# Kernel optimization log

Measured on AMD Instinct MI355X. Metric: run time of the kernel, lower is better.

The kernel has to match this reference:

```python
import math
import jax, jax.numpy as jnp
import numpy as np

B, N, D = 16, 2048, 128
MASK_VALUE = -1000000.0


def setup_inputs() -> dict:
    key = jax.random.key(0)
    k1, k2, k3, k4 = jax.random.split(key, 4)
    queries = jax.random.normal(k1, (B, N, D), dtype=jnp.float32)
    keys = jax.random.normal(k2, (B, N, D), dtype=jnp.float32)
    values = jax.random.normal(k3, (B, N, D), dtype=jnp.float32)
    valid_lens = jax.random.randint(k4, (B,), 0, N, dtype=jnp.int32)
    return {"queries": queries, "keys": keys, "values": values, "valid_lens": valid_lens}


def reference(queries, keys, values, valid_lens):
    d = queries.shape[-1]
    # [B, Nq, Nk] full score matrix, as in the original bmm
    scores = jnp.einsum("bqd,bkd->bqk", queries, keys) / math.sqrt(d)
    # Faithful to the source bug: valid_lens.dim (a method) != 1, so it is
    # flattened and scores[idx][valid_len:] = -1e6 masks QUERY ROWS >= valid_len.
    row_idx = jnp.arange(scores.shape[1])  # [Nq]
    row_mask = row_idx[None, :, None] >= valid_lens[:, None, None]  # [B, Nq, 1]
    scores = jnp.where(row_mask, MASK_VALUE, scores)
    attn = jax.nn.softmax(scores, axis=-1)
    # dropout p=0.0 -> identity
    return jnp.einsum("bqk,bkd->bqd", attn, values)
```

## Files before the change

kernel.cpp:

```cpp
#include <hip/hip_runtime.h>

#define BN 2048
#define DD 128

typedef __attribute__((ext_vector_type(8))) short bf8;
typedef __attribute__((ext_vector_type(16))) float f16v;

__device__ __forceinline__ short bf16rne(float f) {
    unsigned u = __float_as_uint(f);
    u = (u + 0x7FFFu + ((u >> 16) & 1u)) >> 16;
    return (short)u;
}

__launch_bounds__(256, 2)
__global__ void attn_kernel(const float* __restrict__ Q,
                            const float* __restrict__ K,
                            const float* __restrict__ V,
                            const int* __restrict__ VL,
                            float* __restrict__ O) {
    __shared__ short sK[128 * 128];
    __shared__ short sV[128 * 128];
    __shared__ short sP[4 * 32 * 64];

    const int tid  = threadIdx.x;
    const int wave = tid >> 6;
    const int lane = tid & 63;
    const int lw   = lane & 31;
    const int lh   = lane >> 5;
    const int rt   = wave & 1;
    const int kh   = wave >> 1;

    const int L  = blockIdx.x;
    const int b  = (L & 7) | (((L >> 3) & 1) << 3);
    const int qt = L >> 4;
    const int q0 = qt * 64;

    const int vlen = VL[b];

    constexpr float SCL2 = 1.4426950408889634f * 0.08838834764831845f;

    float sclm[16];
    #pragma unroll
    for (int reg = 0; reg < 16; ++reg) {
        int row = (reg & 3) + 8 * (reg >> 2) + 4 * lh;
        int qg = q0 + rt * 32 + row;
        sclm[reg] = (qg >= vlen) ? 0.0f : SCL2;
    }

    const size_t qoff = ((size_t)b * BN + q0 + rt * 32 + lw) * DD;
    bf8 qfrag[8];
    #pragma unroll
    for (int ks = 0; ks < 8; ++ks) {
        int d0 = ks * 16 + lh * 8;
        float4 f0 = *(const float4*)(Q + qoff + d0);
        float4 f1 = *(const float4*)(Q + qoff + d0 + 4);
        bf8 w;
        w[0] = bf16rne(f0.x); w[1] = bf16rne(f0.y);
        w[2] = bf16rne(f0.z); w[3] = bf16rne(f0.w);
        w[4] = bf16rne(f1.x); w[5] = bf16rne(f1.y);
        w[6] = bf16rne(f1.z); w[7] = bf16rne(f1.w);
        qfrag[ks] = w;
    }

    f16v oacc[4] = {};
    float l[16];
    #pragma unroll
    for (int i = 0; i < 16; ++i) l[i] = 0.0f;

    const int pbase = wave * (32 * 64);

    for (int it = 0; it < 16; ++it) {
        const int kb = it * 128;

        {
            int g  = tid & 15;
            int r0 = tid >> 4;
            #pragma unroll
            for (int i = 0; i < 8; ++i) {
                int r = r0 + 16 * i;
                const float* src = K + ((size_t)b * BN + kb + r) * DD + g * 8;
                float4 f0 = *(const float4*)(src);
                float4 f1 = *(const float4*)(src + 4);
                bf8 w;
                w[0] = bf16rne(f0.x); w[1] = bf16rne(f0.y);
                w[2] = bf16rne(f0.z); w[3] = bf16rne(f0.w);
                w[4] = bf16rne(f1.x); w[5] = bf16rne(f1.y);
                w[6] = bf16rne(f1.z); w[7] = bf16rne(f1.w);
                int sg = (g & 8) | ((g ^ r) & 7);
                *(bf8*)&sK[r * 128 + sg * 8] = w;
            }
        }
        {
            int dq  = tid & 31;
            int kg0 = tid >> 5;
            #pragma unroll
            for (int i = 0; i < 2; ++i) {
                int kg = kg0 + 8 * i;
                float vr[32];
                #pragma unroll
                for (int j = 0; j < 8; ++j) {
                    float4 t = *(const float4*)(V + ((size_t)b * BN + kb + kg * 8 + j) * DD + dq * 4);
                    vr[j * 4 + 0] = t.x; vr[j * 4 + 1] = t.y;
                    vr[j * 4 + 2] = t.z; vr[j * 4 + 3] = t.w;
                }
                #pragma unroll
                for (int c = 0; c < 4; ++c) {
                    int d = dq * 4 + c;
                    bf8 w;
                    #pragma unroll
                    for (int j = 0; j < 8; ++j) w[j] = bf16rne(vr[j * 4 + c]);
                    int sg = (kg & 8) | ((kg ^ d) & 7);
                    *(bf8*)&sV[d * 128 + sg * 8] = w;
                }
            }
        }
        __syncthreads();

        f16v s0 = {}, s1 = {};
        #pragma unroll
        for (int ks = 0; ks < 8; ++ks) {
            int g  = ks * 2 + lh;
            int r0 = kh * 64 + lw;
            int sgA = (g & 8) | ((g ^ r0) & 7);
            bf8 b0 = *(const bf8*)&sK[r0 * 128 + sgA * 8];
            s0 = __builtin_amdgcn_mfma_f32_32x32x16_bf16(qfrag[ks], b0, s0, 0, 0, 0);
            int r1 = r0 + 32;
            int sgB = (g & 8) | ((g ^ r1) & 7);
            bf8 b1 = *(const bf8*)&sK[r1 * 128 + sgB * 8];
            s1 = __builtin_amdgcn_mfma_f32_32x32x16_bf16(qfrag[ks], b1, s1, 0, 0, 0);
        }

        #pragma unroll
        for (int reg = 0; reg < 16; ++reg) {
            float p0 = __builtin_amdgcn_exp2f(s0[reg] * sclm[reg]);
            float p1 = __builtin_amdgcn_exp2f(s1[reg] * sclm[reg]);
            l[reg] += p0 + p1;
            int row = (reg & 3) + 8 * (reg >> 2) + 4 * lh;
            int g0 = lw >> 3;
            sP[pbase + row * 64 + ((g0 ^ row) & 7) * 8 + (lw & 7)] = bf16rne(p0);
            int g1 = 4 + (lw >> 3);
            sP[pbase + row * 64 + ((g1 ^ row) & 7) * 8 + (lw & 7)] = bf16rne(p1);
        }

        #pragma unroll
        for (int ks = 0; ks < 4; ++ks) {
            int gk  = ks * 2 + lh;
            int sgp = (gk ^ lw) & 7;
            bf8 pa = *(const bf8*)&sP[pbase + lw * 64 + sgp * 8];
            #pragma unroll
            for (int ot = 0; ot < 4; ++ot) {
                int d   = ot * 32 + lw;
                int gv  = kh * 8 + ks * 2 + lh;
                int sgv = (gv & 8) | ((gv ^ d) & 7);
                bf8 vb = *(const bf8*)&sV[d * 128 + sgv * 8];
                oacc[ot] = __builtin_amdgcn_mfma_f32_32x32x16_bf16(pa, vb, oacc[ot], 0, 0, 0);
            }
        }
        __syncthreads();
    }

    float* oSh = (float*)sK;
    float* lSh = (float*)sV;
    if (kh == 1) {
        #pragma unroll
        for (int ot = 0; ot < 4; ++ot) {
            #pragma unroll
            for (int reg = 0; reg < 16; ++reg) {
                int row = (reg & 3) + 8 * (reg >> 2) + 4 * lh;
                oSh[rt * 4096 + row * 128 + ot * 32 + lw] = oacc[ot][reg];
            }
        }
        #pragma unroll
        for (int reg = 0; reg < 16; ++reg)
            lSh[rt * 1024 + reg * 64 + lane] = l[reg];
    }
    __syncthreads();
    if (kh == 0) {
        #pragma unroll
        for (int reg = 0; reg < 16; ++reg)
            l[reg] += lSh[rt * 1024 + reg * 64 + lane];
        #pragma unroll
        for (int reg = 0; reg < 16; ++reg) {
            float t = l[reg];
            t += __shfl_xor(t, 1, 64);
            t += __shfl_xor(t, 2, 64);
            t += __shfl_xor(t, 4, 64);
            t += __shfl_xor(t, 8, 64);
            t += __shfl_xor(t, 16, 64);
            l[reg] = t;
        }
        #pragma unroll
        for (int ot = 0; ot < 4; ++ot) {
            #pragma unroll
            for (int reg = 0; reg < 16; ++reg) {
                int row = (reg & 3) + 8 * (reg >> 2) + 4 * lh;
                float val = oacc[ot][reg] + oSh[rt * 4096 + row * 128 + ot * 32 + lw];
                val /= l[reg];
                O[((size_t)b * BN + q0 + rt * 32 + row) * DD + ot * 32 + lw] = val;
            }
        }
    }
}

extern "C" void kernel_launch(void* const* d_in, const int* in_sizes, int n_in,
                              void* d_out, int out_size, void* d_ws, size_t ws_size,
                              hipStream_t stream) {
    const float* Q  = (const float*)d_in[0];
    const float* K  = (const float*)d_in[1];
    const float* V  = (const float*)d_in[2];
    const int*   VL = (const int*)d_in[3];
    float* O = (float*)d_out;
    attn_kernel<<<512, 256, 0, stream>>>(Q, K, V, VL, O);
}
```

Baseline: 185.1 us.

## Pre-convert K/V to bf16 fragment layout and stream tiles via LDS DMA

A separate prep kernel converts K and V to bf16 once per call and stores them in the workspace, already laid out as MFMA fragments. The attention kernel then streams each tile into LDS with global_load_lds DMA, double-buffering K and V across iterations. P is passed between lanes by register shuffles instead of through LDS, and each wave now covers all 64 queries over its own key slice, with a cross-wave reduction at the end. This removes the fp32 reload and conversion of K/V that every query block repeated, at the cost of an extra launch, workspace traffic and a slow scalar fallback when the workspace is too small.

```diff
diff --git a/kernel.cpp b/kernel.cpp
--- a/kernel.cpp
+++ b/kernel.cpp
@@ -12,194 +12,263 @@
     return (short)u;
 }
 
+__device__ __forceinline__ unsigned pk2(float a, float b) {
+    return ((unsigned)(unsigned short)bf16rne(b) << 16) | (unsigned short)bf16rne(a);
+}
+
+__device__ __forceinline__ bf8 cvt8(float4 f0, float4 f1) {
+    bf8 w;
+    w[0] = bf16rne(f0.x); w[1] = bf16rne(f0.y);
+    w[2] = bf16rne(f0.z); w[3] = bf16rne(f0.w);
+    w[4] = bf16rne(f1.x); w[5] = bf16rne(f1.y);
+    w[6] = bf16rne(f1.z); w[7] = bf16rne(f1.w);
+    return w;
+}
+
+__device__ __forceinline__ void dma16(const void* gsrc, void* ldst) {
+    __builtin_amdgcn_global_load_lds(
+        (const __attribute__((address_space(1))) void*)gsrc,
+        (__attribute__((address_space(3))) void*)ldst,
+        16, 0, 0);
+}
+
+__device__ __forceinline__ void dma_tile(short* lds, const short* g, int wave, int lane) {
+    const char* gp = (const char*)g + wave * 8192 + lane * 16;
+    char* lp = (char*)lds + wave * 8192 + lane * 16;
+    #pragma unroll
+    for (int c = 0; c < 8; ++c)
+        dma16(gp + c * 1024, lp + c * 1024);
+}
+
+__launch_bounds__(256, 4)
+__global__ void prep_kernel(const float* __restrict__ K, const float* __restrict__ V,
+                            short* __restrict__ KS, short* __restrict__ VS) {
+    __shared__ short tile[128 * 136];
+    const int t = threadIdx.x;
+    const int blk = blockIdx.x;
+    const bool isK = blk < 256;
+    const int bb = isK ? blk : blk - 256;
+    const int b = bb >> 4, it = bb & 15;
+    const float* src = (isK ? K : V) + ((size_t)b * BN + it * 128) * DD;
+
+    #pragma unroll
+    for (int i = 0; i < 8; ++i) {
+        int gid = t + 256 * i;
+        int r = gid >> 4, g = gid & 15;
+        float4 f0 = *(const float4*)(src + r * DD + g * 8);
+        float4 f1 = *(const float4*)(src + r * DD + g * 8 + 4);
+        *(bf8*)&tile[r * 136 + g * 8] = cvt8(f0, f1);
+    }
+    __syncthreads();
+
+    if (isK) {
+        short* dst = KS + (((size_t)b * 16 + it) << 14);
+        #pragma unroll
+        for (int i = 0; i < 8; ++i) {
+            int o = t + 256 * i;
+            int g = o >> 7, r = o & 127;
+            *(bf8*)&dst[o * 8] = *(const bf8*)&tile[r * 136 + g * 8];
+        }
+    } else {
+        short* dst = VS + (((size_t)b * 16 + it) << 14);
+        #pragma unroll
+        for (int i = 0; i < 4; ++i) {
+            int p = t + 256 * i;
+            int kg = p >> 6;
+            int d0 = (p & 63) * 2;
+            bf8 w0, w1;
+            #pragma unroll
+            for (int j = 0; j < 8; ++j) {
+                unsigned u = *(const unsigned*)&tile[(kg * 8 + j) * 136 + d0];
+                w0[j] = (short)(u & 0xFFFF);
+                w1[j] = (short)(u >> 16);
+            }
+            int o = kg * 128 + d0;
+            *(bf8*)&dst[o * 8] = w0;
+            *(bf8*)&dst[(o + 1) * 8] = w1;
+        }
+    }
+}
+
+__device__ __forceinline__ void build_frags(const f16v& s, float scl, float& l,
+                                            bf8 af[2], int lh) {
+    float pv[16];
+    #pragma unroll
+    for (int r = 0; r < 16; ++r) {
+        pv[r] = __builtin_amdgcn_exp2f(s[r] * scl);
+        l += pv[r];
+    }
+    unsigned P2[8];
+    #pragma unroll
+    for (int G = 0; G < 4; ++G) {
+        P2[G * 2 + 0] = pk2(pv[4 * G + 0], pv[4 * G + 1]);
+        P2[G * 2 + 1] = pk2(pv[4 * G + 2], pv[4 * G + 3]);
+    }
+    #pragma unroll
+    for (int s2 = 0; s2 < 2; ++s2) {
+        unsigned send0 = lh ? P2[4 * s2 + 0] : P2[4 * s2 + 2];
+        unsigned send1 = lh ? P2[4 * s2 + 1] : P2[4 * s2 + 3];
+        unsigned r0 = (unsigned)__shfl_xor((int)send0, 32, 64);
+        unsigned r1 = (unsigned)__shfl_xor((int)send1, 32, 64);
+        unsigned own0 = lh ? P2[4 * s2 + 2] : P2[4 * s2 + 0];
+        unsigned own1 = lh ? P2[4 * s2 + 3] : P2[4 * s2 + 1];
+        union { unsigned u[4]; bf8 v; } f;
+        f.u[0] = lh ? r0 : own0;
+        f.u[1] = lh ? r1 : own1;
+        f.u[2] = lh ? own0 : r0;
+        f.u[3] = lh ? own1 : r1;
+        af[s2] = f.v;
+    }
+}
+
 __launch_bounds__(256, 2)
-__global__ void attn_kernel(const float* __restrict__ Q,
-                            const float* __restrict__ K,
-                            const float* __restrict__ V,
-                            const int* __restrict__ VL,
-                            float* __restrict__ O) {
-    __shared__ short sK[128 * 128];
-    __shared__ short sV[128 * 128];
-    __shared__ short sP[4 * 32 * 64];
+__global__ void attn3(const float* __restrict__ Q,
+                      const short* __restrict__ KS,
+                      const short* __restrict__ VS,
+                      const int* __restrict__ VL,
+                      float* __restrict__ O) {
+    __shared__ __align__(16) char smem[65536 + 1024];
+    short* sK = (short*)smem;
+    short* sV = (short*)(smem + 32768);
+    float* lSh = (float*)(smem + 65536);
+    float* buf4 = (float*)smem;
 
     const int tid  = threadIdx.x;
     const int wave = tid >> 6;
     const int lane = tid & 63;
     const int lw   = lane & 31;
     const int lh   = lane >> 5;
-    const int rt   = wave & 1;
-    const int kh   = wave >> 1;
+    const int kq   = wave;
+    const int kt   = kq * 32;
 
     const int L  = blockIdx.x;
     const int b  = (L & 7) | (((L >> 3) & 1) << 3);
-    const int qt = L >> 4;
-    const int q0 = qt * 64;
+    const int qt0 = L >> 4;
+    const int q0 = qt0 * 64;
 
     const int vlen = VL[b];
-
     constexpr float SCL2 = 1.4426950408889634f * 0.08838834764831845f;
 
-    float sclm[16];
-    #pragma unroll
-    for (int reg = 0; reg < 16; ++reg) {
-        int row = (reg & 3) + 8 * (reg >> 2) + 4 * lh;
-        int qg = q0 + rt * 32 + row;
-        sclm[reg] = (qg >= vlen) ? 0.0f : SCL2;
-    }
-
-    const size_t qoff = ((size_t)b * BN + q0 + rt * 32 + lw) * DD;
-    bf8 qfrag[8];
-    #pragma unroll
-    for (int ks = 0; ks < 8; ++ks) {
-        int d0 = ks * 16 + lh * 8;
-        float4 f0 = *(const float4*)(Q + qoff + d0);
-        float4 f1 = *(const float4*)(Q + qoff + d0 + 4);
-        bf8 w;
-        w[0] = bf16rne(f0.x); w[1] = bf16rne(f0.y);
-        w[2] = bf16rne(f0.z); w[3] = bf16rne(f0.w);
-        w[4] = bf16rne(f1.x); w[5] = bf16rne(f1.y);
-        w[6] = bf16rne(f1.z); w[7] = bf16rne(f1.w);
-        qfrag[ks] = w;
-    }
-
-    f16v oacc[4] = {};
-    float l[16];
-    #pragma unroll
-    for (int i = 0; i < 16; ++i) l[i] = 0.0f;
-
-    const int pbase = wave * (32 * 64);
+    const float scl0 = (q0 + lw      >= vlen) ? 0.0f : SCL2;
+    const float scl1 = (q0 + 32 + lw >= vlen) ? 0.0f : SCL2;
+
+    const short* kbase = KS + (((size_t)b * 16) << 14);
+    const short* vbase = VS + (((size_t)b * 16) << 14);
+
+    dma_tile(sK, kbase, wave, lane);
+
+    bf8 qfrag[2][8];
+    #pragma unroll
+    for (int qt = 0; qt < 2; ++qt) {
+        const float* qp = Q + ((size_t)b * BN + q0 + qt * 32 + lw) * DD;
+        #pragma unroll
+        for (int ks = 0; ks < 8; ++ks) {
+            int d0 = ks * 16 + lh * 8;
+            float4 f0 = *(const float4*)(qp + d0);
+            float4 f1 = *(const float4*)(qp + d0 + 4);
+            qfrag[qt][ks] = cvt8(f0, f1);
+        }
+    }
+
+    f16v oacc[2][4] = {};
+    float l0 = 0.0f, l1 = 0.0f;
 
     for (int it = 0; it < 16; ++it) {
-        const int kb = it * 128;
-
-        {
-            int g  = tid & 15;
-            int r0 = tid >> 4;
+        __syncthreads();
+        dma_tile(sV, vbase + ((size_t)it << 14), wave, lane);
+
+        f16v s0 = {}, s1 = {};
+        #pragma unroll
+        for (int ks = 0; ks < 8; ++ks) {
+            const bf8 kf = *(const bf8*)&sK[(((ks * 2 + lh) << 7) + kt + lw) * 8];
+            s0 = __builtin_amdgcn_mfma_f32_32x32x16_bf16(kf, qfrag[0][ks], s0, 0, 0, 0);
+            s1 = __builtin_amdgcn_mfma_f32_32x32x16_bf16(kf, qfrag[1][ks], s1, 0, 0, 0);
+        }
+
+        bf8 af0[2], af1[2];
+        build_frags(s0, scl0, l0, af0, lh);
+        build_frags(s1, scl1, l1, af1, lh);
+
+        __syncthreads();
+        if (it < 15)
+            dma_tile(sK, kbase + ((size_t)(it + 1) << 14), wave, lane);
+
+        #pragma unroll
+        for (int s = 0; s < 2; ++s) {
             #pragma unroll
-            for (int i = 0; i < 8; ++i) {
-                int r = r0 + 16 * i;
-                const float* src = K + ((size_t)b * BN + kb + r) * DD + g * 8;
-                float4 f0 = *(const float4*)(src);
-                float4 f1 = *(const float4*)(src + 4);
-                bf8 w;
-                w[0] = bf16rne(f0.x); w[1] = bf16rne(f0.y);
-                w[2] = bf16rne(f0.z); w[3] = bf16rne(f0.w);
-                w[4] = bf16rne(f1.x); w[5] = bf16rne(f1.y);
-                w[6] = bf16rne(f1.z); w[7] = bf16rne(f1.w);
-                int sg = (g & 8) | ((g ^ r) & 7);
-                *(bf8*)&sK[r * 128 + sg * 8] = w;
+            for (int ot = 0; ot < 4; ++ot) {
+                const bf8 vf = *(const bf8*)&sV[(((kq * 4 + 2 * s + lh) << 7) + ot * 32 + lw) * 8];
+                oacc[0][ot] = __builtin_amdgcn_mfma_f32_32x32x16_bf16(af0[s], vf, oacc[0][ot], 0, 0, 0);
+                oacc[1][ot] = __builtin_amdgcn_mfma_f32_32x32x16_bf16(af1[s], vf, oacc[1][ot], 0, 0, 0);
             }
         }
-        {
-            int dq  = tid & 31;
-            int kg0 = tid >> 5;
+    }
+
+    l0 += __shfl_xor(l0, 32, 64);
+    l1 += __shfl_xor(l1, 32, 64);
+    __syncthreads();
+    if (lh == 0) {
+        lSh[wave * 64 + lw] = l0;
+        lSh[wave * 64 + 32 + lw] = l1;
+    }
+
+    const size_t orow0 = (size_t)b * BN + q0;
+    #pragma unroll
+    for (int half = 0; half < 2; ++half) {
+        #pragma unroll
+        for (int qt = 0; qt < 2; ++qt) {
             #pragma unroll
-            for (int i = 0; i < 2; ++i) {
-                int kg = kg0 + 8 * i;
-                float vr[32];
+            for (int oi = 0; oi < 2; ++oi) {
+                int ot = half * 2 + oi;
                 #pragma unroll
-                for (int j = 0; j < 8; ++j) {
-                    float4 t = *(const float4*)(V + ((size_t)b * BN + kb + kg * 8 + j) * DD + dq * 4);
-                    vr[j * 4 + 0] = t.x; vr[j * 4 + 1] = t.y;
-                    vr[j * 4 + 2] = t.z; vr[j * 4 + 3] = t.w;
-                }
-                #pragma unroll
-                for (int c = 0; c < 4; ++c) {
-                    int d = dq * 4 + c;
-                    bf8 w;
-                    #pragma unroll
-                    for (int j = 0; j < 8; ++j) w[j] = bf16rne(vr[j * 4 + c]);
-                    int sg = (kg & 8) | ((kg ^ d) & 7);
-                    *(bf8*)&sV[d * 128 + sg * 8] = w;
+                for (int reg = 0; reg < 16; ++reg) {
+                    int row = (reg & 3) + 8 * (reg >> 2) + 4 * lh;
+                    buf4[wave * 4096 + (qt * 32 + row) * 64 + oi * 32 + lw] =
+                        oacc[qt][ot][reg];
                 }
             }
         }
         __syncthreads();
-
-        f16v s0 = {}, s1 = {};
-        #pragma unroll
-        for (int ks = 0; ks < 8; ++ks) {
-            int g  = ks * 2 + lh;
-            int r0 = kh * 64 + lw;
-            int sgA = (g & 8) | ((g ^ r0) & 7);
-            bf8 b0 = *(const bf8*)&sK[r0 * 128 + sgA * 8];
-            s0 = __builtin_amdgcn_mfma_f32_32x32x16_bf16(qfrag[ks], b0, s0, 0, 0, 0);
-            int r1 = r0 + 32;
-            int sgB = (g & 8) | ((g ^ r1) & 7);
-            bf8 b1 = *(const bf8*)&sK[r1 * 128 + sgB * 8];
-            s1 = __builtin_amdgcn_mfma_f32_32x32x16_bf16(qfrag[ks], b1, s1, 0, 0, 0);
-        }
-
-        #pragma unroll
-        for (int reg = 0; reg < 16; ++reg) {
-            float p0 = __builtin_amdgcn_exp2f(s0[reg] * sclm[reg]);
-            float p1 = __builtin_amdgcn_exp2f(s1[reg] * sclm[reg]);
-            l[reg] += p0 + p1;
-            int row = (reg & 3) + 8 * (reg >> 2) + 4 * lh;
-            int g0 = lw >> 3;
-            sP[pbase + row * 64 + ((g0 ^ row) & 7) * 8 + (lw & 7)] = bf16rne(p0);
-            int g1 = 4 + (lw >> 3);
-            sP[pbase + row * 64 + ((g1 ^ row) & 7) * 8 + (lw & 7)] = bf16rne(p1);
-        }
-
-        #pragma unroll
-        for (int ks = 0; ks < 4; ++ks) {
-            int gk  = ks * 2 + lh;
-            int sgp = (gk ^ lw) & 7;
-            bf8 pa = *(const bf8*)&sP[pbase + lw * 64 + sgp * 8];
-            #pragma unroll
-            for (int ot = 0; ot < 4; ++ot) {
-                int d   = ot * 32 + lw;
-                int gv  = kh * 8 + ks * 2 + lh;
-                int sgv = (gv & 8) | ((gv ^ d) & 7);
-                bf8 vb = *(const bf8*)&sV[d * 128 + sgv * 8];
-                oacc[ot] = __builtin_amdgcn_mfma_f32_32x32x16_bf16(pa, vb, oacc[ot], 0, 0, 0);
-            }
-        }
-        __syncthreads();
-    }
-
-    float* oSh = (float*)sK;
-    float* lSh = (float*)sV;
-    if (kh == 1) {
-        #pragma unroll
-        for (int ot = 0; ot < 4; ++ot) {
-            #pragma unroll
-            for (int reg = 0; reg < 16; ++reg) {
-                int row = (reg & 3) + 8 * (reg >> 2) + 4 * lh;
-                oSh[rt * 4096 + row * 128 + ot * 32 + lw] = oacc[ot][reg];
-            }
-        }
-        #pragma unroll
-        for (int reg = 0; reg < 16; ++reg)
-            lSh[rt * 1024 + reg * 64 + lane] = l[reg];
-    }
-    __syncthreads();
-    if (kh == 0) {
-        #pragma unroll
-        for (int reg = 0; reg < 16; ++reg)
-            l[reg] += lSh[rt * 1024 + reg * 64 + lane];
-        #pragma unroll
-        for (int reg = 0; reg < 16; ++reg) {
-            float t = l[reg];
-            t += __shfl_xor(t, 1, 64);
-            t += __shfl_xor(t, 2, 64);
-            t += __shfl_xor(t, 4, 64);
-            t += __shfl_xor(t, 8, 64);
-            t += __shfl_xor(t, 16, 64);
-            l[reg] = t;
-        }
-        #pragma unroll
-        for (int ot = 0; ot < 4; ++ot) {
-            #pragma unroll
-            for (int reg = 0; reg < 16; ++reg) {
-                int row = (reg & 3) + 8 * (reg >> 2) + 4 * lh;
-                float val = oacc[ot][reg] + oSh[rt * 4096 + row * 128 + ot * 32 + lw];
-                val /= l[reg];
-                O[((size_t)b * BN + q0 + rt * 32 + row) * DD + ot * 32 + lw] = val;
-            }
-        }
-    }
+        #pragma unroll
+        for (int i = 0; i < 16; ++i) {
+            int q = wave * 16 + i;
+            float ltot = lSh[q] + lSh[64 + q] + lSh[128 + q] + lSh[192 + q];
+            float rinv = __builtin_amdgcn_rcpf(ltot);
+            float v = buf4[q * 64 + lane] + buf4[4096 + q * 64 + lane] +
+                      buf4[8192 + q * 64 + lane] + buf4[12288 + q * 64 + lane];
+            O[(orow0 + q) * DD + half * 64 + lane] = v * rinv;
+        }
+        __syncthreads();
+    }
+}
+
+__launch_bounds__(256, 2)
+__global__ void attn_fallback(const float* __restrict__ Q,
+                              const float* __restrict__ K,
+                              const float* __restrict__ V,
+                              const int* __restrict__ VL,
+                              float* __restrict__ O) {
+    const int b = blockIdx.x >> 7;
+    const int q = ((blockIdx.x & 127) * 16) + (threadIdx.x >> 4);
+    const int dl = (threadIdx.x & 15) * 8;
+    const int vlen = VL[b];
+    const float scl = (q >= vlen) ? 0.0f : (1.4426950408889634f * 0.08838834764831845f);
+    const float* qp = Q + ((size_t)b * BN + q) * DD;
+    float acc[8] = {};
+    float l = 0.0f;
+    for (int k = 0; k < BN; ++k) {
+        const float* kp = K + ((size_t)b * BN + k) * DD;
+        float s = 0.0f;
+        for (int d = 0; d < DD; ++d) s += qp[d] * kp[d];
+        float p = __builtin_amdgcn_exp2f(s * scl);
+        l += p;
+        const float* vp = V + ((size_t)b * BN + k) * DD + dl;
+        #pragma unroll
+        for (int e = 0; e < 8; ++e) acc[e] += p * vp[e];
+    }
+    float* op = O + ((size_t)b * BN + q) * DD + dl;
+    #pragma unroll
+    for (int e = 0; e < 8; ++e) op[e] = acc[e] / l;
 }
 
 extern "C" void kernel_launch(void* const* d_in, const int* in_sizes, int n_in,
@@ -210,5 +279,14 @@
     const float* V  = (const float*)d_in[2];
     const int*   VL = (const int*)d_in[3];
     float* O = (float*)d_out;
-    attn_kernel<<<512, 256, 0, stream>>>(Q, K, V, VL, O);
-}
+
+    const size_t need = (size_t)2 * 16 * 16 * 16384 * sizeof(short);
+    if (ws_size >= need) {
+        short* KS = (short*)d_ws;
+        short* VS = KS + (size_t)16 * 16 * 16384;
+        prep_kernel<<<512, 256, 0, stream>>>(K, V, KS, VS);
+        attn3<<<512, 256, 0, stream>>>(Q, KS, VS, VL, O);
+    } else {
+        attn_fallback<<<2048, 256, 0, stream>>>(Q, K, V, VL, O);
+    }
+}
```

New measurement: 148.6 us. -19.8%, faster.
